# Kernel tuning notes

Hardware: AMD Instinct MI355X
Metric: run time of the kernel (lower is better)

## Reference

```python
import jax, jax.numpy as jnp
import numpy as np

NUM_HEADS = 16


def setup_inputs() -> dict:
    key = jax.random.key(0)
    k1, k2, k3 = jax.random.split(key, 3)
    B, S, D = 4, 2048, 1024
    hidden_states = jax.random.normal(k1, (B, S, D), dtype=jnp.float32)
    w_qkv = jax.random.normal(k2, (D, 3 * D), dtype=jnp.float32) * (1.0 / np.sqrt(D))
    w_out = jax.random.normal(k3, (D, D), dtype=jnp.float32) * (1.0 / np.sqrt(D))
    return {"hidden_states": hidden_states, "w_qkv": w_qkv, "w_out": w_out}


def reference(hidden_states, w_qkv, w_out):
    B, S, D = hidden_states.shape
    H = NUM_HEADS
    d = D // H
    # fused QKV projection: [B, S, 3D] -> [3, B, S, H, d]
    qkv = (hidden_states @ w_qkv).reshape(B, S, 3, H, d)
    q, k, v = jnp.moveaxis(qkv, 2, 0)  # each [B, S, H, d]
    scale = 1.0 / np.sqrt(d).astype(np.float32)
    scores = jnp.einsum("bqhd,bkhd->bhqk", q, k) * scale  # [B, H, S, S]
    attn = jax.nn.softmax(scores, axis=-1)
    ctx = jnp.einsum("bhqk,bkhd->bqhd", attn, v).reshape(B, S, D)
    return ctx @ w_out
```

## Files before the change

kernel.cpp:

```cpp
#include <hip/hip_runtime.h>
#include <hip/hip_bf16.h>
#include <math.h>

typedef __bf16 bf16;
typedef __bf16 bf16x4 __attribute__((ext_vector_type(4)));
typedef __bf16 bf16x8 __attribute__((ext_vector_type(8)));
typedef float  f32x4  __attribute__((ext_vector_type(4)));

#define B_  4
#define S_  2048
#define D_  1024
#define H_  16
#define DH  64
#define M_  (B_*S_)
#define BH_ (B_*H_)

#define QSCALE 0.18033688011112042f

__device__ __forceinline__ void glds16(const bf16* g, bf16* l) {
  __builtin_amdgcn_global_load_lds((const __attribute__((address_space(1))) void*)g,
                                   (__attribute__((address_space(3))) void*)l, 16, 0, 0);
}

__global__ void cvt_f32_bf16(const float* __restrict__ in, bf16* __restrict__ out, int n) {
  int i = (blockIdx.x * 256 + threadIdx.x) * 4;
  if (i < n) {
    float4 v = *(const float4*)(in + i);
    bf16x4 o = { (bf16)v.x, (bf16)v.y, (bf16)v.z, (bf16)v.w };
    *(bf16x4*)(out + i) = o;
  }
}

__global__ void transpose_cvt2(const float* __restrict__ wqkv, const float* __restrict__ wout,
                               bf16* __restrict__ wqkvT, bf16* __restrict__ woutT) {
  __shared__ float tile[32][33];
  int bx = blockIdx.x;
  const float* in; bf16* out; int C, c0;
  if (bx < 96) { in = wqkv; out = wqkvT; C = 3072; c0 = bx * 32; }
  else         { in = wout; out = woutT; C = 1024; c0 = (bx - 96) * 32; }
  int tx = threadIdx.x, ty = threadIdx.y;
  int r0 = blockIdx.y * 32;
  #pragma unroll
  for (int i = ty; i < 32; i += 8) tile[i][tx] = in[(size_t)(r0 + i) * C + c0 + tx];
  __syncthreads();
  #pragma unroll
  for (int i = ty; i < 32; i += 8) out[(size_t)(c0 + i) * D_ + r0 + tx] = (bf16)tile[tx][i];
}

#define LDA2 32

__device__ __forceinline__ void gemm_core(const bf16* __restrict__ A, const bf16* __restrict__ Bt,
                                          int m0, int n0, bf16* As, bf16* Bs,
                                          int tid, f32x4 acc[4][4]) {
  int wave = tid >> 6, lane = tid & 63, quad = lane >> 4, l16 = lane & 15;
  int wm = (wave >> 1) * 64, wn = (wave & 1) * 64;
  int lr = lane >> 2, lc = (lane & 3) * 8;
  const bf16* gA = A  + (size_t)(m0 + wave * 32 + lr) * D_ + lc;
  const bf16* gB = Bt + (size_t)(n0 + wave * 32 + lr) * D_ + lc;
  bf16* lA = As + wave * 32 * LDA2;
  bf16* lB = Bs + wave * 32 * LDA2;
  for (int k0 = 0; k0 < D_; k0 += 32) {
    glds16(gA + k0,           lA);
    glds16(gA + k0 + 16 * D_, lA + 16 * LDA2);
    glds16(gB + k0,           lB);
    glds16(gB + k0 + 16 * D_, lB + 16 * LDA2);
    __syncthreads();
    bf16x8 af[4], bff[4];
    #pragma unroll
    for (int i = 0; i < 4; i++) af[i]  = *(const bf16x8*)(As + (wm + i * 16 + l16) * LDA2 + quad * 8);
    #pragma unroll
    for (int j = 0; j < 4; j++) bff[j] = *(const bf16x8*)(Bs + (wn + j * 16 + l16) * LDA2 + quad * 8);
    #pragma unroll
    for (int i = 0; i < 4; i++)
      #pragma unroll
      for (int j = 0; j < 4; j++)
        acc[i][j] = __builtin_amdgcn_mfma_f32_16x16x32_bf16(af[i], bff[j], acc[i][j], 0, 0, 0);
    __syncthreads();
  }
}

__global__ __launch_bounds__(256) void gemm_qkv(const bf16* __restrict__ A, const bf16* __restrict__ Bt,
                                                bf16* __restrict__ Qb, bf16* __restrict__ Kb,
                                                bf16* __restrict__ Vtb) {
  __shared__ __attribute__((aligned(16))) bf16 As[128 * LDA2];
  __shared__ __attribute__((aligned(16))) bf16 Bs[128 * LDA2];
  int tid = threadIdx.x;
  int m0 = blockIdx.y * 128, n0 = blockIdx.x * 128;
  f32x4 acc[4][4] = {};
  gemm_core(A, Bt, m0, n0, As, Bs, tid, acc);
  int wave = tid >> 6, lane = tid & 63, quad = lane >> 4, l16 = lane & 15;
  int wm = (wave >> 1) * 64, wn = (wave & 1) * 64;
  int which = n0 >> 10;
  if (which == 2) {
    #pragma unroll
    for (int i = 0; i < 4; i++) {
      int mb = m0 + wm + i * 16 + quad * 4;
      int b = mb >> 11, s = mb & 2047;
      #pragma unroll
      for (int j = 0; j < 4; j++) {
        int n = n0 + wn + j * 16 + l16;
        int h = (n >> 6) & 15, dd = n & 63;
        bf16x4 v4 = { (bf16)acc[i][j][0], (bf16)acc[i][j][1], (bf16)acc[i][j][2], (bf16)acc[i][j][3] };
        *(bf16x4*)(Vtb + ((size_t)(b * H_ + h) * DH + dd) * S_ + s) = v4;
      }
    }
  } else {
    bf16* dst = (which == 0) ? Qb : Kb;
    float sc = (which == 0) ? QSCALE : 1.0f;
    #pragma unroll
    for (int i = 0; i < 4; i++) {
      #pragma unroll
      for (int j = 0; j < 4; j++) {
        int n = n0 + wn + j * 16 + l16;
        int h = (n >> 6) & 15, dd = n & 63;
        #pragma unroll
        for (int r = 0; r < 4; r++) {
          int m = m0 + wm + i * 16 + quad * 4 + r;
          int b = m >> 11, s = m & 2047;
          dst[(((size_t)(b * H_ + h)) * S_ + s) * DH + dd] = (bf16)(acc[i][j][r] * sc);
        }
      }
    }
  }
}

__global__ __launch_bounds__(256) void gemm_out(const bf16* __restrict__ A, const bf16* __restrict__ Bt,
                                                float* __restrict__ C) {
  __shared__ __attribute__((aligned(16))) bf16 As[128 * LDA2];
  __shared__ __attribute__((aligned(16))) bf16 Bs[128 * LDA2];
  int tid = threadIdx.x;
  int m0 = blockIdx.y * 128, n0 = blockIdx.x * 128;
  f32x4 acc[4][4] = {};
  gemm_core(A, Bt, m0, n0, As, Bs, tid, acc);
  int wave = tid >> 6, lane = tid & 63, quad = lane >> 4, l16 = lane & 15;
  int wm = (wave >> 1) * 64, wn = (wave & 1) * 64;
  #pragma unroll
  for (int i = 0; i < 4; i++)
    #pragma unroll
    for (int j = 0; j < 4; j++) {
      int n = n0 + wn + j * 16 + l16;
      #pragma unroll
      for (int r = 0; r < 4; r++) {
        int m = m0 + wm + i * 16 + quad * 4 + r;
        C[(size_t)m * D_ + n] = acc[i][j][r];
      }
    }
}

#define LDK 72
#define LDP 40

__global__ __launch_bounds__(256, 2) void attn(const bf16* __restrict__ Qb, const bf16* __restrict__ Kb,
                                               const bf16* __restrict__ Vtb, bf16* __restrict__ ctx) {
  __shared__ __attribute__((aligned(16))) bf16 Ks[64 * LDK];
  __shared__ __attribute__((aligned(16))) bf16 Vs[64 * LDK];
  __shared__ __attribute__((aligned(16))) bf16 Ps[4][64 * LDP];
  int tid = threadIdx.x;
  int wave = tid >> 6, lane = tid & 63, quad = lane >> 4, l16 = lane & 15;
  int bh = blockIdx.y;
  int b = bh >> 4, h = bh & 15;
  int q0 = blockIdx.x * 256 + wave * 64;
  const bf16* Qp = Qb  + (size_t)bh * S_ * DH;
  const bf16* Kp = Kb  + (size_t)bh * S_ * DH;
  const bf16* Vp = Vtb + (size_t)bh * DH * S_;

  bf16x8 qf[4][2];
  #pragma unroll
  for (int nq = 0; nq < 4; nq++)
    #pragma unroll
    for (int ks = 0; ks < 2; ks++)
      qf[nq][ks] = *(const bf16x8*)(Qp + (size_t)(q0 + nq * 16 + l16) * DH + ks * 32 + quad * 8);

  bf16 one1 = (bf16)1.0f;
  bf16x8 onesf = { one1, one1, one1, one1, one1, one1, one1, one1 };

  f32x4 o[4][4] = {};
  f32x4 oden[4] = {};

  for (int kt = 0; kt < S_ / 64; kt++) {
    #pragma unroll
    for (int c = tid; c < 512; c += 256) {
      int row = c >> 3, cc = (c & 7) << 3;
      *(bf16x8*)(Ks + row * LDK + cc) = *(const bf16x8*)(Kp + (size_t)(kt * 64 + row) * DH + cc);
      *(bf16x8*)(Vs + row * LDK + cc) = *(const bf16x8*)(Vp + (size_t)row * S_ + kt * 64 + cc);
    }
    __syncthreads();

    bf16x8 vf[4][2];
    #pragma unroll
    for (int td = 0; td < 4; td++)
      #pragma unroll
      for (int ks = 0; ks < 2; ks++)
        vf[td][ks] = *(const bf16x8*)(Vs + (td * 16 + l16) * LDK + ks * 32 + quad * 8);

    #pragma unroll
    for (int hh = 0; hh < 2; hh++) {
      #pragma unroll
      for (int kq2 = 0; kq2 < 2; kq2++) {
        int kq = hh * 2 + kq2;
        bf16x8 kfr[2];
        #pragma unroll
        for (int ks = 0; ks < 2; ks++)
          kfr[ks] = *(const bf16x8*)(Ks + (kq * 16 + l16) * LDK + ks * 32 + quad * 8);
        #pragma unroll
        for (int nq = 0; nq < 4; nq++) {
          f32x4 st = {};
          st = __builtin_amdgcn_mfma_f32_16x16x32_bf16(kfr[0], qf[nq][0], st, 0, 0, 0);
          st = __builtin_amdgcn_mfma_f32_16x16x32_bf16(kfr[1], qf[nq][1], st, 0, 0, 0);
          bf16x4 pk;
          #pragma unroll
          for (int r = 0; r < 4; r++) pk[r] = (bf16)__builtin_amdgcn_exp2f(st[r]);
          *(bf16x4*)(&Ps[wave][(nq * 16 + l16) * LDP + kq2 * 16 + quad * 4]) = pk;
        }
      }
      #pragma unroll
      for (int nq = 0; nq < 4; nq++) {
        bf16x8 pf = *(const bf16x8*)(&Ps[wave][(nq * 16 + l16) * LDP + quad * 8]);
        oden[nq] = __builtin_amdgcn_mfma_f32_16x16x32_bf16(pf, onesf, oden[nq], 0, 0, 0);
        #pragma unroll
        for (int td = 0; td < 4; td++)
          o[nq][td] = __builtin_amdgcn_mfma_f32_16x16x32_bf16(pf, vf[td][hh], o[nq][td], 0, 0, 0);
      }
    }
    __syncthreads();
  }

  #pragma unroll
  for (int nq = 0; nq < 4; nq++) {
    #pragma unroll
    for (int r = 0; r < 4; r++) {
      float inv = 1.0f / oden[nq][r];
      int q = q0 + nq * 16 + quad * 4 + r;
      #pragma unroll
      for (int td = 0; td < 4; td++) {
        int dd = td * 16 + l16;
        ctx[((size_t)(b * S_) + q) * D_ + h * DH + dd] = (bf16)(o[nq][td][r] * inv);
      }
    }
  }
}

extern "C" void kernel_launch(void* const* d_in, const int* in_sizes, int n_in,
                              void* d_out, int out_size, void* d_ws, size_t ws_size,
                              hipStream_t stream) {
  (void)in_sizes; (void)n_in; (void)out_size; (void)ws_size;
  const float* hidden = (const float*)d_in[0];
  const float* w_qkv  = (const float*)d_in[1];
  const float* w_out  = (const float*)d_in[2];
  float* out = (float*)d_out;

  char* ws = (char*)d_ws;
  size_t off = 0;
  bf16* hb    = (bf16*)(ws + off); off += (size_t)M_ * D_ * 2;
  bf16* wqkvT = (bf16*)(ws + off); off += (size_t)3 * D_ * D_ * 2;
  bf16* woutT = (bf16*)(ws + off); off += (size_t)D_ * D_ * 2;
  bf16* Qb    = (bf16*)(ws + off); off += (size_t)M_ * D_ * 2;
  bf16* Kb    = (bf16*)(ws + off); off += (size_t)M_ * D_ * 2;
  bf16* Vtb   = (bf16*)(ws + off); off += (size_t)M_ * D_ * 2;
  bf16* ctxb  = hb;

  cvt_f32_bf16<<<(M_ * D_ / 4 + 255) / 256, 256, 0, stream>>>(hidden, hb, M_ * D_);
  transpose_cvt2<<<dim3(128, D_ / 32), dim3(32, 8), 0, stream>>>(w_qkv, w_out, wqkvT, woutT);
  gemm_qkv<<<dim3(3 * D_ / 128, M_ / 128), 256, 0, stream>>>(hb, wqkvT, Qb, Kb, Vtb);
  attn<<<dim3(S_ / 256, BH_), 256, 0, stream>>>(Qb, Kb, Vtb, ctxb);
  gemm_out<<<dim3(D_ / 128, M_ / 128), 256, 0, stream>>>(ctxb, woutT, out);
}
```

Measured before the change: 274.4 us.

## Double-buffer K/V tiles in attention via register prefetch and swap grid order

The attention kernel now keeps two shared-memory buffers for K and V. The next tile is loaded into registers before the current tile's MFMA work and written to the other buffer afterwards, which leaves one barrier per iteration instead of two. The launch grid is also swapped so blockIdx.x walks batch-heads and blockIdx.y walks query blocks, which changes which blocks run together and may affect L2 reuse of K/V. In exchange it uses more LDS and more registers, which could reduce occupancy.

```diff
diff --git a/kernel.cpp b/kernel.cpp
--- a/kernel.cpp
+++ b/kernel.cpp
@@ -149,21 +149,24 @@
 
 #define LDK 72
 #define LDP 40
+#define NT  (S_ / 64)
 
 __global__ __launch_bounds__(256, 2) void attn(const bf16* __restrict__ Qb, const bf16* __restrict__ Kb,
                                                const bf16* __restrict__ Vtb, bf16* __restrict__ ctx) {
-  __shared__ __attribute__((aligned(16))) bf16 Ks[64 * LDK];
-  __shared__ __attribute__((aligned(16))) bf16 Vs[64 * LDK];
+  __shared__ __attribute__((aligned(16))) bf16 Ks[2][64 * LDK];
+  __shared__ __attribute__((aligned(16))) bf16 Vs[2][64 * LDK];
   __shared__ __attribute__((aligned(16))) bf16 Ps[4][64 * LDP];
   int tid = threadIdx.x;
   int wave = tid >> 6, lane = tid & 63, quad = lane >> 4, l16 = lane & 15;
-  int bh = blockIdx.y;
+  int bh = blockIdx.x;
   int b = bh >> 4, h = bh & 15;
-  int q0 = blockIdx.x * 256 + wave * 64;
+  int q0 = blockIdx.y * 256 + wave * 64;
   const bf16* Qp = Qb  + (size_t)bh * S_ * DH;
   const bf16* Kp = Kb  + (size_t)bh * S_ * DH;
   const bf16* Vp = Vtb + (size_t)bh * DH * S_;
 
+  int srow = tid >> 3, scc = (tid & 7) << 3;
+
   bf16x8 qf[4][2];
   #pragma unroll
   for (int nq = 0; nq < 4; nq++)
@@ -177,21 +180,37 @@
   f32x4 o[4][4] = {};
   f32x4 oden[4] = {};
 
-  for (int kt = 0; kt < S_ / 64; kt++) {
-    #pragma unroll
-    for (int c = tid; c < 512; c += 256) {
-      int row = c >> 3, cc = (c & 7) << 3;
-      *(bf16x8*)(Ks + row * LDK + cc) = *(const bf16x8*)(Kp + (size_t)(kt * 64 + row) * DH + cc);
-      *(bf16x8*)(Vs + row * LDK + cc) = *(const bf16x8*)(Vp + (size_t)row * S_ + kt * 64 + cc);
-    }
+  {
+    bf16x8 k0a = *(const bf16x8*)(Kp + (size_t)srow * DH + scc);
+    bf16x8 k0b = *(const bf16x8*)(Kp + (size_t)(32 + srow) * DH + scc);
+    bf16x8 v0a = *(const bf16x8*)(Vp + (size_t)srow * S_ + scc);
+    bf16x8 v0b = *(const bf16x8*)(Vp + (size_t)(32 + srow) * S_ + scc);
+    *(bf16x8*)(Ks[0] + srow * LDK + scc)        = k0a;
+    *(bf16x8*)(Ks[0] + (32 + srow) * LDK + scc) = k0b;
+    *(bf16x8*)(Vs[0] + srow * LDK + scc)        = v0a;
+    *(bf16x8*)(Vs[0] + (32 + srow) * LDK + scc) = v0b;
+  }
+
+  for (int kt = 0; kt < NT; kt++) {
+    int cur = kt & 1;
     __syncthreads();
 
+    bf16x8 ka, kb2, va, vb;
+    if (kt + 1 < NT) {
+      const bf16* Kn = Kp + (size_t)(kt + 1) * 64 * DH;
+      const bf16* Vn = Vp + (size_t)(kt + 1) * 64;
+      ka  = *(const bf16x8*)(Kn + (size_t)srow * DH + scc);
+      kb2 = *(const bf16x8*)(Kn + (size_t)(32 + srow) * DH + scc);
+      va  = *(const bf16x8*)(Vn + (size_t)srow * S_ + scc);
+      vb  = *(const bf16x8*)(Vn + (size_t)(32 + srow) * S_ + scc);
+    }
+
     bf16x8 vf[4][2];
     #pragma unroll
     for (int td = 0; td < 4; td++)
       #pragma unroll
       for (int ks = 0; ks < 2; ks++)
-        vf[td][ks] = *(const bf16x8*)(Vs + (td * 16 + l16) * LDK + ks * 32 + quad * 8);
+        vf[td][ks] = *(const bf16x8*)(Vs[cur] + (td * 16 + l16) * LDK + ks * 32 + quad * 8);
 
     #pragma unroll
     for (int hh = 0; hh < 2; hh++) {
@@ -201,7 +220,7 @@
         bf16x8 kfr[2];
         #pragma unroll
         for (int ks = 0; ks < 2; ks++)
-          kfr[ks] = *(const bf16x8*)(Ks + (kq * 16 + l16) * LDK + ks * 32 + quad * 8);
+          kfr[ks] = *(const bf16x8*)(Ks[cur] + (kq * 16 + l16) * LDK + ks * 32 + quad * 8);
         #pragma unroll
         for (int nq = 0; nq < 4; nq++) {
           f32x4 st = {};
@@ -222,7 +241,14 @@
           o[nq][td] = __builtin_amdgcn_mfma_f32_16x16x32_bf16(pf, vf[td][hh], o[nq][td], 0, 0, 0);
       }
     }
-    __syncthreads();
+
+    if (kt + 1 < NT) {
+      int nxt = cur ^ 1;
+      *(bf16x8*)(Ks[nxt] + srow * LDK + scc)        = ka;
+      *(bf16x8*)(Ks[nxt] + (32 + srow) * LDK + scc) = kb2;
+      *(bf16x8*)(Vs[nxt] + srow * LDK + scc)        = va;
+      *(bf16x8*)(Vs[nxt] + (32 + srow) * LDK + scc) = vb;
+    }
   }
 
   #pragma unroll
@@ -262,6 +288,6 @@
   cvt_f32_bf16<<<(M_ * D_ / 4 + 255) / 256, 256, 0, stream>>>(hidden, hb, M_ * D_);
   transpose_cvt2<<<dim3(128, D_ / 32), dim3(32, 8), 0, stream>>>(w_qkv, w_out, wqkvT, woutT);
   gemm_qkv<<<dim3(3 * D_ / 128, M_ / 128), 256, 0, stream>>>(hb, wqkvT, Qb, Kb, Vtb);
-  attn<<<dim3(S_ / 256, BH_), 256, 0, stream>>>(Qb, Kb, Vtb, ctxb);
+  attn<<<dim3(BH_, S_ / 256), 256, 0, stream>>>(Qb, Kb, Vtb, ctxb);
   gemm_out<<<dim3(D_ / 128, M_ / 128), 256, 0, stream>>>(ctxb, woutT, out);
 }
```

After: 266.3 us. -3.0%, faster.
